# Performance work log

Measured on AMD Instinct MI355X. Metric: run time of the kernel, lower is better.

## Reference

```python
import jax, jax.numpy as jnp
import numpy as np

B, H, L, D = 4, 16, 8192, 64


def setup_inputs() -> dict:
    key = jax.random.key(0)
    ks = jax.random.split(key, 10)
    q = jax.random.normal(ks[0], (B, H, L, D), dtype=jnp.float32)
    k = jax.random.normal(ks[1], (B, H, L, D), dtype=jnp.float32)
    v = jax.random.normal(ks[2], (B, H, L, D), dtype=jnp.float32)
    mask = jax.random.randint(ks[3], (B, H, L), 0, 2, dtype=jnp.int32)
    s = 1.0 / np.sqrt(D)
    Wa_w = jax.random.uniform(ks[4], (D, D), jnp.float32, -s, s)  # torch Linear weight [out,in]
    Wa_b = jax.random.uniform(ks[5], (D,), jnp.float32, -s, s)
    Ua_w = jax.random.uniform(ks[6], (D, D), jnp.float32, -s, s)
    Ua_b = jax.random.uniform(ks[7], (D,), jnp.float32, -s, s)
    va_w = jax.random.uniform(ks[8], (1, D), jnp.float32, -s, s)
    va_b = jax.random.uniform(ks[9], (1,), jnp.float32, -s, s)
    return {"q": q, "k": k, "v": v, "mask": mask,
            "Wa_w": Wa_w, "Wa_b": Wa_b, "Ua_w": Ua_w, "Ua_b": Ua_b,
            "va_w": va_w, "va_b": va_b}


def reference(q, k, v, mask, Wa_w, Wa_b, Ua_w, Ua_b, va_w, va_b):
    # e1 = Wa(q), e2 = Ua(k)  (torch Linear: x @ W.T + b)
    e1 = jnp.einsum('bhld,ed->bhle', q, Wa_w) + Wa_b
    e2 = jnp.einsum('bhld,ed->bhle', k, Ua_w) + Ua_b
    t = jnp.tanh(e1 + e2)
    # va: [B,H,L,D] -> [B,H,L]
    e = jnp.einsum('bhld,d->bhl', t, va_w[0]) + va_b[0]
    e = jnp.where(mask == 0, jnp.float32(-10000.0), e)
    alpha = jax.nn.softmax(e, axis=-1)  # softmax over sequence length
    return alpha[..., None] * v
```

## Files before the change

kernel.cpp:

```cpp
#include <hip/hip_runtime.h>
#include <hip/hip_bf16.h>

#define BH   64
#define LSEQ 8192
#define DDIM 64
#define NPOS (BH * LSEQ)
#define NT4  (NPOS * DDIM / 4)

typedef __attribute__((ext_vector_type(8))) short bf16x8;
typedef __attribute__((ext_vector_type(4))) float f32x4;

__device__ inline short f2bf(float f) {
    __bf16 b = (__bf16)f;
    return __builtin_bit_cast(short, b);
}
__device__ inline float bf2f(short s) {
    unsigned u = ((unsigned)(unsigned short)s) << 16;
    return __builtin_bit_cast(float, u);
}
__device__ inline void split8(const float* f, bf16x8& hi, bf16x8& lo) {
#pragma unroll
    for (int j = 0; j < 8; j++) {
        short h = f2bf(f[j]);
        hi[j] = h;
        lo[j] = f2bf(f[j] - bf2f(h));
    }
}
__device__ inline float tanh_fast(float x) {
    float ex = __expf(2.f * x);
    return 1.f - 2.f * __builtin_amdgcn_rcpf(ex + 1.f);
}

__global__ __launch_bounds__(256, 3) void score_kernel(
    const float* __restrict__ q, const float* __restrict__ k,
    const int*   __restrict__ mask,
    const float* __restrict__ Waw, const float* __restrict__ Wab,
    const float* __restrict__ Uaw, const float* __restrict__ Uab,
    const float* __restrict__ vaw, const float* __restrict__ vab_p,
    float* __restrict__ e_out)
{
    const int lane = threadIdx.x & 63;
    const int m    = lane & 15;
    const int quad = lane >> 4;
    const int wgl  = blockIdx.x * 4 + (threadIdx.x >> 6);
    const long t0  = (long)wgl * 4;

    bf16x8 bwa[4][2], bua[4][2];
    float bias_s[4], vav[4];
    float vab;

    float4 A[8], B[8];
    int4 mkA, mkB;

    auto issue = [&](float4 (&buf)[8], int4& mk, long tile) {
        mk = ((const int4*)mask)[tile * 4 + quad];
        const size_t off = (size_t)(tile * 16 + m) * 64 + quad * 8;
        buf[0] = *((const float4*)(q + off));
        buf[1] = *((const float4*)(q + off + 4));
        buf[2] = *((const float4*)(k + off));
        buf[3] = *((const float4*)(k + off + 4));
        buf[4] = *((const float4*)(q + off + 32));
        buf[5] = *((const float4*)(q + off + 36));
        buf[6] = *((const float4*)(k + off + 32));
        buf[7] = *((const float4*)(k + off + 36));
    };

    auto load_weights = [&]() {
#pragma unroll
        for (int t = 0; t < 4; t++) {
            const int n = t * 16 + m;
            bias_s[t] = Wab[n] + Uab[n];
            vav[t]    = vaw[n];
#pragma unroll
            for (int s = 0; s < 2; s++) {
                const int k0 = s * 32 + quad * 8;
                const float4 wA = ((const float4*)(Waw + n * 64 + k0))[0];
                const float4 wB = ((const float4*)(Waw + n * 64 + k0))[1];
                const float4 uA = ((const float4*)(Uaw + n * 64 + k0))[0];
                const float4 uB = ((const float4*)(Uaw + n * 64 + k0))[1];
                float wf[8] = {wA.x, wA.y, wA.z, wA.w, wB.x, wB.y, wB.z, wB.w};
                float uf[8] = {uA.x, uA.y, uA.z, uA.w, uB.x, uB.y, uB.z, uB.w};
                bf16x8 wv, uv;
#pragma unroll
                for (int j = 0; j < 8; j++) { wv[j] = f2bf(wf[j]); uv[j] = f2bf(uf[j]); }
                bwa[t][s] = wv;
                bua[t][s] = uv;
            }
        }
        vab = vab_p[0];
    };

    auto compute = [&](const float4 (&buf)[8], const int4& mk, long tile) {
        f32x4 acc[4];
#pragma unroll
        for (int t = 0; t < 4; t++) acc[t] = (f32x4){0.f, 0.f, 0.f, 0.f};
#pragma unroll
        for (int s = 0; s < 2; s++) {
            const float4 qa = buf[s * 4 + 0], qb = buf[s * 4 + 1];
            const float4 ka = buf[s * 4 + 2], kb = buf[s * 4 + 3];
            float qf[8] = {qa.x, qa.y, qa.z, qa.w, qb.x, qb.y, qb.z, qb.w};
            float kf[8] = {ka.x, ka.y, ka.z, ka.w, kb.x, kb.y, kb.z, kb.w};
            bf16x8 qhi, qlo, khi, klo;
            split8(qf, qhi, qlo);
            split8(kf, khi, klo);
#pragma unroll
            for (int t = 0; t < 4; t++) {
                acc[t] = __builtin_amdgcn_mfma_f32_16x16x32_bf16(qhi, bwa[t][s], acc[t], 0, 0, 0);
                acc[t] = __builtin_amdgcn_mfma_f32_16x16x32_bf16(qlo, bwa[t][s], acc[t], 0, 0, 0);
                acc[t] = __builtin_amdgcn_mfma_f32_16x16x32_bf16(khi, bua[t][s], acc[t], 0, 0, 0);
                acc[t] = __builtin_amdgcn_mfma_f32_16x16x32_bf16(klo, bua[t][s], acc[t], 0, 0, 0);
            }
        }
        float c[4] = {0.f, 0.f, 0.f, 0.f};
#pragma unroll
        for (int t = 0; t < 4; t++) {
#pragma unroll
            for (int r = 0; r < 4; r++)
                c[r] += vav[t] * tanh_fast(acc[t][r] + bias_s[t]);
        }
#pragma unroll
        for (int r = 0; r < 4; r++) {
#pragma unroll
            for (int off2 = 1; off2 < 16; off2 <<= 1)
                c[r] += __shfl_xor(c[r], off2, 16);
        }
        if (m == 0) {
            float4 ev;
            ev.x = mk.x ? c[0] + vab : -10000.f;
            ev.y = mk.y ? c[1] + vab : -10000.f;
            ev.z = mk.z ? c[2] + vab : -10000.f;
            ev.w = mk.w ? c[3] + vab : -10000.f;
            *((float4*)(e_out + tile * 16 + quad * 4)) = ev;
        }
    };

    issue(A, mkA, t0 + 0);
    issue(B, mkB, t0 + 1);
    __builtin_amdgcn_sched_barrier(0);
    load_weights();
    __builtin_amdgcn_sched_barrier(0);
    compute(A, mkA, t0 + 0);
    issue(A, mkA, t0 + 2);
    __builtin_amdgcn_sched_barrier(0);
    compute(B, mkB, t0 + 1);
    issue(B, mkB, t0 + 3);
    __builtin_amdgcn_sched_barrier(0);
    compute(A, mkA, t0 + 2);
    compute(B, mkB, t0 + 3);
}

__global__ __launch_bounds__(1024) void rowstat_kernel(
    const float* __restrict__ e, float* __restrict__ stats)
{
    const int row = blockIdx.x;
    const size_t base = (size_t)row * LSEQ;
    const int tid  = threadIdx.x;
    const int lane = tid & 63;
    const int wv   = tid >> 6;
    __shared__ float redmax[16];
    __shared__ float redsum[16];

    float4 e0 = ((const float4*)(e + base))[tid];
    float4 e1 = ((const float4*)(e + base))[1024 + tid];
    float em[8] = {e0.x, e0.y, e0.z, e0.w, e1.x, e1.y, e1.z, e1.w};

    float lm = em[0];
#pragma unroll
    for (int j = 1; j < 8; j++) lm = fmaxf(lm, em[j]);
#pragma unroll
    for (int off = 32; off >= 1; off >>= 1) lm = fmaxf(lm, __shfl_xor(lm, off, 64));
    if (lane == 0) redmax[wv] = lm;
    __syncthreads();
    float M = redmax[0];
#pragma unroll
    for (int i = 1; i < 16; i++) M = fmaxf(M, redmax[i]);

    float ls = 0.f;
#pragma unroll
    for (int j = 0; j < 8; j++) ls += __expf(em[j] - M);
#pragma unroll
    for (int off = 32; off >= 1; off >>= 1) ls += __shfl_xor(ls, off, 64);
    if (lane == 0) redsum[wv] = ls;
    __syncthreads();
    if (tid == 0) {
        float S = 0.f;
#pragma unroll
        for (int i = 0; i < 16; i++) S += redsum[i];
        stats[row * 2]     = M;
        stats[row * 2 + 1] = 1.f / S;
    }
}

__global__ __launch_bounds__(256) void scale_kernel(
    const float* __restrict__ v, const float* __restrict__ e,
    const float* __restrict__ stats, float* __restrict__ out)
{
    const size_t b0 = (size_t)blockIdx.x * 1024 + threadIdx.x;
    const f32x4* vp = (const f32x4*)v;
    f32x4*       op = (f32x4*)out;

    size_t idx[4];
    f32x4  vv[4];
    float  ee[4];
    float2 st[4];
#pragma unroll
    for (int j = 0; j < 4; j++) {
        idx[j] = b0 + (size_t)j * 256;
        vv[j]  = __builtin_nontemporal_load(vp + idx[j]);
    }
#pragma unroll
    for (int j = 0; j < 4; j++) {
        const size_t p = idx[j] >> 4;
        ee[j] = e[p];
        st[j] = ((const float2*)stats)[p >> 13];
    }
#pragma unroll
    for (int j = 0; j < 4; j++) {
        const float a = __expf(ee[j] - st[j].x) * st[j].y;
        f32x4 o = vv[j] * a;
        __builtin_nontemporal_store(o, op + idx[j]);
    }
}

extern "C" void kernel_launch(void* const* d_in, const int* in_sizes, int n_in,
                              void* d_out, int out_size, void* d_ws, size_t ws_size,
                              hipStream_t stream) {
    const float* q    = (const float*)d_in[0];
    const float* k    = (const float*)d_in[1];
    const float* v    = (const float*)d_in[2];
    const int*   mask = (const int*)d_in[3];
    const float* Waw  = (const float*)d_in[4];
    const float* Wab  = (const float*)d_in[5];
    const float* Uaw  = (const float*)d_in[6];
    const float* Uab  = (const float*)d_in[7];
    const float* vaw  = (const float*)d_in[8];
    const float* vab  = (const float*)d_in[9];
    float* out = (float*)d_out;

    float* e_buf = (float*)d_ws;
    float* stats = (float*)d_ws + NPOS;

    score_kernel<<<2048, 256, 0, stream>>>(q, k, mask, Waw, Wab, Uaw, Uab, vaw, vab, e_buf);
    rowstat_kernel<<<BH, 1024, 0, stream>>>(e_buf, stats);
    scale_kernel<<<NT4 / 1024, 256, 0, stream>>>(v, e_buf, stats, out);
}
```

Baseline: 423.9 us.

## Stage q/k tiles through swizzled LDS with fully coalesced global loads

```diff
diff --git a/kernel.cpp b/kernel.cpp
--- a/kernel.cpp
+++ b/kernel.cpp
@@ -31,7 +31,7 @@
     return 1.f - 2.f * __builtin_amdgcn_rcpf(ex + 1.f);
 }
 
-__global__ __launch_bounds__(256, 3) void score_kernel(
+__global__ __launch_bounds__(64, 2) void score_kernel(
     const float* __restrict__ q, const float* __restrict__ k,
     const int*   __restrict__ mask,
     const float* __restrict__ Waw, const float* __restrict__ Wab,
@@ -39,30 +39,40 @@
     const float* __restrict__ vaw, const float* __restrict__ vab_p,
     float* __restrict__ e_out)
 {
-    const int lane = threadIdx.x & 63;
+    const int lane = threadIdx.x;
     const int m    = lane & 15;
-    const int quad = lane >> 4;
-    const int wgl  = blockIdx.x * 4 + (threadIdx.x >> 6);
-    const long t0  = (long)wgl * 4;
+    const int g    = lane >> 4;
+    const long t0  = (long)blockIdx.x * 4;
+
+    __shared__ float lds[2][2048];
 
     bf16x8 bwa[4][2], bua[4][2];
     float bias_s[4], vav[4];
     float vab;
 
-    float4 A[8], B[8];
-    int4 mkA, mkB;
-
-    auto issue = [&](float4 (&buf)[8], int4& mk, long tile) {
-        mk = ((const int4*)mask)[tile * 4 + quad];
-        const size_t off = (size_t)(tile * 16 + m) * 64 + quad * 8;
-        buf[0] = *((const float4*)(q + off));
-        buf[1] = *((const float4*)(q + off + 4));
-        buf[2] = *((const float4*)(k + off));
-        buf[3] = *((const float4*)(k + off + 4));
-        buf[4] = *((const float4*)(q + off + 32));
-        buf[5] = *((const float4*)(q + off + 36));
-        buf[6] = *((const float4*)(k + off + 32));
-        buf[7] = *((const float4*)(k + off + 36));
+    float4 RA[8], RB[8];
+    int4 mk0, mk1, mk2, mk3;
+
+    auto gload = [&](float4 (&R)[8], int4& mk, long tile) {
+        mk = ((const int4*)mask)[tile * 4 + g];
+        const float* qb = q + tile * 1024;
+        const float* kb = k + tile * 1024;
+#pragma unroll
+        for (int i = 0; i < 4; i++)
+            R[i]     = *((const float4*)(qb + i * 256 + lane * 4));
+#pragma unroll
+        for (int i = 0; i < 4; i++)
+            R[4 + i] = *((const float4*)(kb + i * 256 + lane * 4));
+    };
+
+    auto stage = [&](const float4 (&R)[8], int buf) {
+#pragma unroll
+        for (int i = 0; i < 8; i++) {
+            const int row  = 4 * (i & 3) + g;
+            const int half = i >> 2;
+            float* dst = &lds[buf][half * 1024 + row * 64 + ((m ^ (row & 7)) << 2)];
+            *((float4*)dst) = R[i];
+        }
     };
 
     auto load_weights = [&]() {
@@ -73,7 +83,7 @@
             vav[t]    = vaw[n];
 #pragma unroll
             for (int s = 0; s < 2; s++) {
-                const int k0 = s * 32 + quad * 8;
+                const int k0 = s * 32 + g * 8;
                 const float4 wA = ((const float4*)(Waw + n * 64 + k0))[0];
                 const float4 wB = ((const float4*)(Waw + n * 64 + k0))[1];
                 const float4 uA = ((const float4*)(Uaw + n * 64 + k0))[0];
@@ -90,14 +100,18 @@
         vab = vab_p[0];
     };
 
-    auto compute = [&](const float4 (&buf)[8], const int4& mk, long tile) {
+    auto compute = [&](int buf, const int4& mk, long tile) {
         f32x4 acc[4];
 #pragma unroll
         for (int t = 0; t < 4; t++) acc[t] = (f32x4){0.f, 0.f, 0.f, 0.f};
+        const float* L = lds[buf];
 #pragma unroll
         for (int s = 0; s < 2; s++) {
-            const float4 qa = buf[s * 4 + 0], qb = buf[s * 4 + 1];
-            const float4 ka = buf[s * 4 + 2], kb = buf[s * 4 + 3];
+            const int c0 = s * 8 + g * 2;
+            const float4 qa = *((const float4*)(L + m * 64 + (( c0      ^ (m & 7)) << 2)));
+            const float4 qb = *((const float4*)(L + m * 64 + (((c0 + 1) ^ (m & 7)) << 2)));
+            const float4 ka = *((const float4*)(L + 1024 + m * 64 + (( c0      ^ (m & 7)) << 2)));
+            const float4 kb = *((const float4*)(L + 1024 + m * 64 + (((c0 + 1) ^ (m & 7)) << 2)));
             float qf[8] = {qa.x, qa.y, qa.z, qa.w, qb.x, qb.y, qb.z, qb.w};
             float kf[8] = {ka.x, ka.y, ka.z, ka.w, kb.x, kb.y, kb.z, kb.w};
             bf16x8 qhi, qlo, khi, klo;
@@ -130,23 +144,23 @@
             ev.y = mk.y ? c[1] + vab : -10000.f;
             ev.z = mk.z ? c[2] + vab : -10000.f;
             ev.w = mk.w ? c[3] + vab : -10000.f;
-            *((float4*)(e_out + tile * 16 + quad * 4)) = ev;
-        }
-    };
-
-    issue(A, mkA, t0 + 0);
-    issue(B, mkB, t0 + 1);
-    __builtin_amdgcn_sched_barrier(0);
+            *((float4*)(e_out + tile * 16 + g * 4)) = ev;
+        }
+    };
+
+    gload(RA, mk0, t0 + 0);
+    gload(RB, mk1, t0 + 1);
     load_weights();
-    __builtin_amdgcn_sched_barrier(0);
-    compute(A, mkA, t0 + 0);
-    issue(A, mkA, t0 + 2);
-    __builtin_amdgcn_sched_barrier(0);
-    compute(B, mkB, t0 + 1);
-    issue(B, mkB, t0 + 3);
-    __builtin_amdgcn_sched_barrier(0);
-    compute(A, mkA, t0 + 2);
-    compute(B, mkB, t0 + 3);
+    stage(RA, 0);
+    gload(RA, mk2, t0 + 2);
+    stage(RB, 1);
+    gload(RB, mk3, t0 + 3);
+    compute(0, mk0, t0 + 0);
+    stage(RA, 0);
+    compute(1, mk1, t0 + 1);
+    stage(RB, 1);
+    compute(0, mk2, t0 + 2);
+    compute(1, mk3, t0 + 3);
 }
 
 __global__ __launch_bounds__(1024) void rowstat_kernel(
@@ -240,7 +254,7 @@
     float* e_buf = (float*)d_ws;
     float* stats = (float*)d_ws + NPOS;
 
-    score_kernel<<<2048, 256, 0, stream>>>(q, k, mask, Waw, Wab, Uaw, Uab, vaw, vab, e_buf);
+    score_kernel<<<NPOS / 64, 64, 0, stream>>>(q, k, mask, Waw, Wab, Uaw, Uab, vaw, vab, e_buf);
     rowstat_kernel<<<BH, 1024, 0, stream>>>(e_buf, stats);
     scale_kernel<<<NT4 / 1024, 256, 0, stream>>>(v, e_buf, stats, out);
 }
```

Result: slower. 472.4 us (+11.4%).
